# Performance work log

Hardware: AMD Instinct MI355X
Metric: run time of the kernel (lower is better)

Reference implementation:

```python
import jax, jax.numpy as jnp
import numpy as np

NBITS = 4
QN = -(2 ** (NBITS - 1))      # -8
QP = 2 ** (NBITS - 1) - 1     # 7


def grad_scale(x, scale):
    # forward: x ; backward: grad * scale (LSQ gradient scaling)
    return x * scale + jax.lax.stop_gradient(x * (1.0 - scale))


def round_pass(x):
    # straight-through estimator for round
    return x + jax.lax.stop_gradient(jnp.round(x) - x)


def lsq_quant_weight(w, alpha):
    g = 1.0 / jnp.sqrt(jnp.float32(w.size * QP))
    a = grad_scale(alpha, g)
    return round_pass(jnp.clip(w / a, QN, QP)) * a


def setup_inputs() -> dict:
    key = jax.random.key(0)
    k = jax.random.split(key, 5)
    C = 256
    N = 262144
    x = jax.random.normal(k[0], (N, C), dtype=jnp.float32)
    w1 = jax.random.normal(k[1], (C, C), dtype=jnp.float32) * 0.02
    b1 = jnp.zeros((C,), dtype=jnp.float32)
    w2 = jax.random.normal(k[2], (C, C), dtype=jnp.float32) * 0.02
    b2 = jnp.zeros((C,), dtype=jnp.float32)
    # LSQ alpha init: 2 * mean|w| / sqrt(Qp)
    alpha1 = 2.0 * jnp.mean(jnp.abs(w1)) / jnp.sqrt(jnp.float32(QP))
    alpha2 = 2.0 * jnp.mean(jnp.abs(w2)) / jnp.sqrt(jnp.float32(QP))
    return {"x": x, "w1": w1, "b1": b1, "alpha1": alpha1,
            "w2": w2, "b2": b2, "alpha2": alpha2}


def reference(x, w1, b1, alpha1, w2, b2, alpha2):
    # fc1 (4-bit LSQ weight quant) -> ReLU -> fc2 (4-bit LSQ) -> Sigmoid
    wq1 = lsq_quant_weight(w1, alpha1)
    h = jax.nn.relu(x @ wq1.T + b1)           # [N, C]
    wq2 = lsq_quant_weight(w2, alpha2)
    return jax.nn.sigmoid(h @ wq2.T + b2)     # [N, C]
```

## Files before the change

kernel.cpp:

```cpp
#include <hip/hip_runtime.h>

typedef __attribute__((ext_vector_type(4))) float f32x4;
typedef __attribute__((ext_vector_type(8))) short bf16x8;

static __device__ __forceinline__ unsigned short f2bf(float f) {
  union { float f; unsigned int u; } v;
  v.f = f;
  unsigned int r = v.u + 0x7fffu + ((v.u >> 16) & 1u);
  return (unsigned short)(r >> 16);
}

static __device__ __forceinline__ void gload16(const void* g, void* l) {
  __builtin_amdgcn_global_load_lds(
      (const __attribute__((address_space(1))) unsigned int*)g,
      (__attribute__((address_space(3))) unsigned int*)l, 16, 0, 0);
}

__global__ void lsq_pack(const float* __restrict__ w1, const float* __restrict__ a1,
                         const float* __restrict__ w2, const float* __restrict__ a2,
                         unsigned short* __restrict__ pq)
{
  int g = blockIdx.x * 256 + threadIdx.x;
  int gg = g & 8191;
  const float* w = (g < 8192) ? w1 : w2;
  float alpha = (g < 8192) ? *a1 : *a2;
  unsigned short* dst = pq + ((g < 8192) ? 0 : 65536);
  int l  = gg & 63;
  int ks = (gg >> 6) & 7;
  int cf = gg >> 9;
  int n  = cf * 16 + (l & 15);
  int kb = ks * 32 + (l >> 4) * 8;
  const float* src = w + n * 256 + kb;
  unsigned short e[8];
  #pragma unroll
  for (int j = 0; j < 8; ++j) {
    float q = src[j] / alpha;
    q = fminf(fmaxf(q, -8.f), 7.f);
    q = rintf(q) * alpha;
    e[j] = f2bf(q);
  }
  uint4 o;
  o.x = e[0] | ((unsigned)e[1] << 16);
  o.y = e[2] | ((unsigned)e[3] << 16);
  o.z = e[4] | ((unsigned)e[5] << 16);
  o.w = e[6] | ((unsigned)e[7] << 16);
  int di = (g < 8192) ? ((cf * 8 + ks) * 64 + l) : ((ks * 16 + cf) * 64 + l);
  *(uint4*)(dst + di * 8) = o;
}

__global__ __launch_bounds__(512, 2) void lsq_fused(
    const float* __restrict__ x, const unsigned short* __restrict__ pqw,
    const float* __restrict__ b1, const float* __restrict__ b2,
    float* __restrict__ out, int ntiles)
{
  __shared__ __align__(16) char w1lds[2][16384];
  __shared__ __align__(16) char w2lds[2][16384];
  __shared__ __align__(16) char hlds[8][2048];

  const int tid  = threadIdx.x;
  const int lane = tid & 63;
  const int w    = tid >> 6;
  const int l15  = lane & 15;
  const int l4   = lane >> 4;
  const int swz  = (l15 & 3) << 4;
  const char* pq1 = (const char*)pqw;
  const char* pq2 = (const char*)pqw + 131072;
  const int wb = w * 1024;
  const int lo = wb + lane * 16;

  gload16(pq1 + lo,        &w1lds[0][0]    + wb);
  gload16(pq1 + 8192 + lo, &w1lds[0][8192] + wb);
  gload16(pq2 + lo,        &w2lds[0][0]    + wb);
  gload16(pq2 + 8192 + lo, &w2lds[0][8192] + wb);
  __syncthreads();

  int gr = 0;
  for (int t = blockIdx.x; t < ntiles; t += gridDim.x) {
    const int rowbase = t * 256 + w * 32;

    bf16x8 xf[2][8];
    #pragma unroll
    for (int g = 0; g < 2; ++g) {
      const float* xp = x + (size_t)(rowbase + g * 16 + l15) * 256 + l4 * 8;
      #pragma unroll
      for (int ks = 0; ks < 8; ++ks) {
        f32x4 r0 = *(const f32x4*)(xp + ks * 32);
        f32x4 r1 = *(const f32x4*)(xp + ks * 32 + 4);
        bf16x8 b;
        #pragma unroll
        for (int j = 0; j < 4; ++j) {
          b[j]     = (short)f2bf(r0[j]);
          b[j + 4] = (short)f2bf(r1[j]);
        }
        xf[g][ks] = b;
      }
    }

    f32x4 acc2[2][16];
    const f32x4 fzero = {0.f, 0.f, 0.f, 0.f};
    #pragma unroll
    for (int g = 0; g < 2; ++g)
      #pragma unroll
      for (int c = 0; c < 16; ++c)
        acc2[g][c] = fzero;

    for (int r = 0; r < 8; ++r) {
      const int cb = gr & 1;
      const int nb = cb ^ 1;
      const int nc = (gr + 1) & 7;
      gload16(pq1 + nc * 16384 + lo,        &w1lds[nb][0]    + wb);
      gload16(pq1 + nc * 16384 + 8192 + lo, &w1lds[nb][8192] + wb);
      gload16(pq2 + nc * 16384 + lo,        &w2lds[nb][0]    + wb);
      gload16(pq2 + nc * 16384 + 8192 + lo, &w2lds[nb][8192] + wb);

      #pragma unroll
      for (int c = 0; c < 2; ++c) {
        f32x4 a0 = fzero, a1v = fzero;
        #pragma unroll
        for (int ks = 0; ks < 8; ++ks) {
          bf16x8 wf = *(const bf16x8*)(&w1lds[cb][0] + c * 8192 + ks * 1024 + lane * 16);
          a0  = __builtin_amdgcn_mfma_f32_16x16x32_bf16(wf, xf[0][ks], a0, 0, 0, 0);
          a1v = __builtin_amdgcn_mfma_f32_16x16x32_bf16(wf, xf[1][ks], a1v, 0, 0, 0);
        }
        const int cf = 2 * r + c;
        f32x4 bv = *(const f32x4*)(b1 + cf * 16 + l4 * 4);
        const int hb = (c * 32 + l4 * 8) ^ swz;
        {
          float v0 = a0[0] + bv[0]; v0 = v0 > 0.f ? v0 : 0.f;
          float v1 = a0[1] + bv[1]; v1 = v1 > 0.f ? v1 : 0.f;
          float v2 = a0[2] + bv[2]; v2 = v2 > 0.f ? v2 : 0.f;
          float v3 = a0[3] + bv[3]; v3 = v3 > 0.f ? v3 : 0.f;
          uint2 o;
          o.x = f2bf(v0) | ((unsigned)f2bf(v1) << 16);
          o.y = f2bf(v2) | ((unsigned)f2bf(v3) << 16);
          *(uint2*)(&hlds[w][0] + l15 * 64 + hb) = o;
        }
        {
          float v0 = a1v[0] + bv[0]; v0 = v0 > 0.f ? v0 : 0.f;
          float v1 = a1v[1] + bv[1]; v1 = v1 > 0.f ? v1 : 0.f;
          float v2 = a1v[2] + bv[2]; v2 = v2 > 0.f ? v2 : 0.f;
          float v3 = a1v[3] + bv[3]; v3 = v3 > 0.f ? v3 : 0.f;
          uint2 o;
          o.x = f2bf(v0) | ((unsigned)f2bf(v1) << 16);
          o.y = f2bf(v2) | ((unsigned)f2bf(v3) << 16);
          *(uint2*)(&hlds[w][0] + (16 + l15) * 64 + hb) = o;
        }
      }
      __builtin_amdgcn_sched_barrier(0);

      bf16x8 hf0 = *(const bf16x8*)(&hlds[w][0] + l15 * 64        + ((l4 * 16) ^ swz));
      bf16x8 hf1 = *(const bf16x8*)(&hlds[w][0] + (16 + l15) * 64 + ((l4 * 16) ^ swz));
      #pragma unroll
      for (int c2 = 0; c2 < 16; ++c2) {
        bf16x8 wf2 = *(const bf16x8*)(&w2lds[cb][0] + c2 * 1024 + lane * 16);
        acc2[0][c2] = __builtin_amdgcn_mfma_f32_16x16x32_bf16(wf2, hf0, acc2[0][c2], 0, 0, 0);
        acc2[1][c2] = __builtin_amdgcn_mfma_f32_16x16x32_bf16(wf2, hf1, acc2[1][c2], 0, 0, 0);
      }
      ++gr;
      __syncthreads();
    }

    #pragma unroll
    for (int g = 0; g < 2; ++g) {
      float* op = out + (size_t)(rowbase + g * 16 + l15) * 256 + l4 * 4;
      #pragma unroll
      for (int c2 = 0; c2 < 16; ++c2) {
        f32x4 bv = *(const f32x4*)(b2 + c2 * 16 + l4 * 4);
        f32x4 o;
        #pragma unroll
        for (int j = 0; j < 4; ++j) {
          float z = acc2[g][c2][j] + bv[j];
          o[j] = 1.f / (1.f + __expf(-z));
        }
        *(f32x4*)(op + c2 * 16) = o;
      }
    }
  }
}

extern "C" void kernel_launch(void* const* d_in, const int* in_sizes, int n_in,
                              void* d_out, int out_size, void* d_ws, size_t ws_size,
                              hipStream_t stream)
{
  const float* x  = (const float*)d_in[0];
  const float* w1 = (const float*)d_in[1];
  const float* b1 = (const float*)d_in[2];
  const float* a1 = (const float*)d_in[3];
  const float* w2 = (const float*)d_in[4];
  const float* b2 = (const float*)d_in[5];
  const float* a2 = (const float*)d_in[6];
  float* out = (float*)d_out;

  unsigned short* pq = (unsigned short*)d_ws;

  long long totalRows = (long long)in_sizes[0] / 256;
  int ntiles = (int)(totalRows / 256);

  lsq_pack<<<64, 256, 0, stream>>>(w1, a1, w2, a2, pq);

  int grid = ntiles < 256 ? ntiles : 256;
  lsq_fused<<<grid, 512, 0, stream>>>(x, pq, b1, b2, out, ntiles);
}
```

Before: 196.3 us.

## Prefetch next x tile into LDS and pass hidden activations via bpermute

The fused MLP kernel now stages the next 128-row x tile into a 128KB LDS buffer with swizzled async global-to-LDS loads, interleaved with the per-chunk weight loads, so HBM reads of x overlap the MFMA work of the current tile. Block size drops to 256 threads at one block per CU, and weight slots are split into a w1 slot and a w2 slot with explicit vmcnt waits and barriers. The ReLU output is moved into the second GEMM's operand layout with ds_bpermute instead of a round trip through LDS. Biases are hoisted into registers. The cost is fewer waves per CU, a large LDS footprint and a more fragile hand-written wait and barrier schedule.

```diff
diff --git a/kernel.cpp b/kernel.cpp
--- a/kernel.cpp
+++ b/kernel.cpp
@@ -2,6 +2,7 @@
 
 typedef __attribute__((ext_vector_type(4))) float f32x4;
 typedef __attribute__((ext_vector_type(8))) short bf16x8;
+typedef __attribute__((ext_vector_type(4))) unsigned int u32x4;
 
 static __device__ __forceinline__ unsigned short f2bf(float f) {
   union { float f; unsigned int u; } v;
@@ -9,12 +10,18 @@
   unsigned int r = v.u + 0x7fffu + ((v.u >> 16) & 1u);
   return (unsigned short)(r >> 16);
 }
-
+static __device__ __forceinline__ unsigned packbf(float a, float b) {
+  return (unsigned)f2bf(a) | ((unsigned)f2bf(b) << 16);
+}
 static __device__ __forceinline__ void gload16(const void* g, void* l) {
   __builtin_amdgcn_global_load_lds(
       (const __attribute__((address_space(1))) unsigned int*)g,
       (__attribute__((address_space(3))) unsigned int*)l, 16, 0, 0);
 }
+
+#define SBAR()   __builtin_amdgcn_s_barrier()
+#define SCHED0() __builtin_amdgcn_sched_barrier(0)
+#define WAITVM(N) do { asm volatile("s_waitcnt vmcnt(" #N ")" ::: "memory"); SCHED0(); } while (0)
 
 __global__ void lsq_pack(const float* __restrict__ w1, const float* __restrict__ a1,
                          const float* __restrict__ w2, const float* __restrict__ a2,
@@ -48,44 +55,50 @@
   *(uint4*)(dst + di * 8) = o;
 }
 
-__global__ __launch_bounds__(512, 2) void lsq_fused(
+__global__ __launch_bounds__(256, 1) void lsq_fused(
     const float* __restrict__ x, const unsigned short* __restrict__ pqw,
     const float* __restrict__ b1, const float* __restrict__ b2,
     float* __restrict__ out, int ntiles)
 {
-  __shared__ __align__(16) char w1lds[2][16384];
-  __shared__ __align__(16) char w2lds[2][16384];
-  __shared__ __align__(16) char hlds[8][2048];
+  __shared__ __align__(16) char lds[163840];
+  char* const xbuf  = lds;
+  char* const slot0 = lds + 131072;
+  char* const slot1 = lds + 147456;
 
   const int tid  = threadIdx.x;
   const int lane = tid & 63;
   const int w    = tid >> 6;
   const int l15  = lane & 15;
   const int l4   = lane >> 4;
-  const int swz  = (l15 & 3) << 4;
   const char* pq1 = (const char*)pqw;
   const char* pq2 = (const char*)pqw + 131072;
-  const int wb = w * 1024;
-  const int lo = wb + lane * 16;
-
-  gload16(pq1 + lo,        &w1lds[0][0]    + wb);
-  gload16(pq1 + 8192 + lo, &w1lds[0][8192] + wb);
-  gload16(pq2 + lo,        &w2lds[0][0]    + wb);
-  gload16(pq2 + 8192 + lo, &w2lds[0][8192] + wb);
-  __syncthreads();
-
-  int gr = 0;
-  for (int t = blockIdx.x; t < ntiles; t += gridDim.x) {
-    const int rowbase = t * 256 + w * 32;
-
-    bf16x8 xf[2][8];
+  const int G = gridDim.x;
+  const f32x4 fz = {0.f, 0.f, 0.f, 0.f};
+
+  f32x4 bA0[8], bA1[8], bB[16];
+  #pragma unroll
+  for (int r = 0; r < 8; ++r) {
+    bA0[r] = *(const f32x4*)(b1 + r * 32 + l4 * 4);
+    bA1[r] = *(const f32x4*)(b1 + r * 32 + 16 + l4 * 4);
+  }
+  #pragma unroll
+  for (int c2 = 0; c2 < 16; ++c2) bB[c2] = *(const f32x4*)(b2 + c2 * 16 + l4 * 4);
+
+  int idx[4];
+  #pragma unroll
+  for (int wi = 0; wi < 4; ++wi)
+    idx[wi] = (((l4 & 1) * 2 + (wi >> 1)) * 16 + l15) * 4;
+
+  bf16x8 xf[2][8];
+  auto CONVERT = [&]() {
     #pragma unroll
     for (int g = 0; g < 2; ++g) {
-      const float* xp = x + (size_t)(rowbase + g * 16 + l15) * 256 + l4 * 8;
+      const int row = w * 32 + g * 16 + l15;
+      const int swz = (l15 & 7) << 4;
       #pragma unroll
       for (int ks = 0; ks < 8; ++ks) {
-        f32x4 r0 = *(const f32x4*)(xp + ks * 32);
-        f32x4 r1 = *(const f32x4*)(xp + ks * 32 + 4);
+        f32x4 r0 = *(const f32x4*)(xbuf + row * 1024 + ((ks * 128 + l4 * 32) ^ swz));
+        f32x4 r1 = *(const f32x4*)(xbuf + row * 1024 + ((ks * 128 + l4 * 32 + 16) ^ swz));
         bf16x8 b;
         #pragma unroll
         for (int j = 0; j < 4; ++j) {
@@ -95,86 +108,130 @@
         xf[g][ks] = b;
       }
     }
-
-    f32x4 acc2[2][16];
-    const f32x4 fzero = {0.f, 0.f, 0.f, 0.f};
-    #pragma unroll
-    for (int g = 0; g < 2; ++g)
-      #pragma unroll
-      for (int c = 0; c < 16; ++c)
-        acc2[g][c] = fzero;
-
+  };
+
+  int t = blockIdx.x;
+
+  {
+    const char* xg = (const char*)x + (size_t)t * 131072;
+    #pragma unroll
+    for (int q = 0; q < 32; ++q) {
+      const int row = q * 4 + w;
+      gload16(xg + row * 1024 + ((lane * 16) ^ ((row & 7) << 4)), xbuf + row * 1024);
+    }
+    #pragma unroll
+    for (int i = 0; i < 4; ++i) {
+      const int sub = i * 4 + w;
+      gload16(pq1 + sub * 1024 + lane * 16, slot0 + sub * 1024);
+    }
+  }
+  WAITVM(0);
+  SBAR();
+  CONVERT();
+  SBAR();
+
+  f32x4 acc2[2][16];
+  #pragma unroll
+  for (int g = 0; g < 2; ++g)
+    #pragma unroll
+    for (int c2 = 0; c2 < 16; ++c2) acc2[g][c2] = fz;
+
+  for (;;) {
+    const int tn = (t + G < ntiles) ? (t + G) : t;
+    const char* xgn = (const char*)x + (size_t)tn * 131072;
+
+    #pragma unroll
     for (int r = 0; r < 8; ++r) {
-      const int cb = gr & 1;
-      const int nb = cb ^ 1;
-      const int nc = (gr + 1) & 7;
-      gload16(pq1 + nc * 16384 + lo,        &w1lds[nb][0]    + wb);
-      gload16(pq1 + nc * 16384 + 8192 + lo, &w1lds[nb][8192] + wb);
-      gload16(pq2 + nc * 16384 + lo,        &w2lds[nb][0]    + wb);
-      gload16(pq2 + nc * 16384 + 8192 + lo, &w2lds[nb][8192] + wb);
-
-      #pragma unroll
-      for (int c = 0; c < 2; ++c) {
-        f32x4 a0 = fzero, a1v = fzero;
+      bf16x8 hf[2];
+      if (r > 0) { WAITVM(2); SBAR(); }
+      #pragma unroll
+      for (int i = 0; i < 4; ++i) {
+        const int sub = i * 4 + w;
+        gload16(pq2 + r * 16384 + sub * 1024 + lane * 16, slot1 + sub * 1024);
+      }
+      SCHED0();
+      #pragma unroll
+      for (int e = 0; e < 2; ++e) {
+        const int row = (r * 4 + e) * 4 + w;
+        gload16(xgn + row * 1024 + ((lane * 16) ^ ((row & 7) << 4)), xbuf + row * 1024);
+      }
+      f32x4 aA[2][2] = {{fz, fz}, {fz, fz}};
+      #pragma unroll
+      for (int c = 0; c < 2; ++c)
         #pragma unroll
         for (int ks = 0; ks < 8; ++ks) {
-          bf16x8 wf = *(const bf16x8*)(&w1lds[cb][0] + c * 8192 + ks * 1024 + lane * 16);
-          a0  = __builtin_amdgcn_mfma_f32_16x16x32_bf16(wf, xf[0][ks], a0, 0, 0, 0);
-          a1v = __builtin_amdgcn_mfma_f32_16x16x32_bf16(wf, xf[1][ks], a1v, 0, 0, 0);
-        }
-        const int cf = 2 * r + c;
-        f32x4 bv = *(const f32x4*)(b1 + cf * 16 + l4 * 4);
-        const int hb = (c * 32 + l4 * 8) ^ swz;
-        {
-          float v0 = a0[0] + bv[0]; v0 = v0 > 0.f ? v0 : 0.f;
-          float v1 = a0[1] + bv[1]; v1 = v1 > 0.f ? v1 : 0.f;
-          float v2 = a0[2] + bv[2]; v2 = v2 > 0.f ? v2 : 0.f;
-          float v3 = a0[3] + bv[3]; v3 = v3 > 0.f ? v3 : 0.f;
-          uint2 o;
-          o.x = f2bf(v0) | ((unsigned)f2bf(v1) << 16);
-          o.y = f2bf(v2) | ((unsigned)f2bf(v3) << 16);
-          *(uint2*)(&hlds[w][0] + l15 * 64 + hb) = o;
-        }
-        {
-          float v0 = a1v[0] + bv[0]; v0 = v0 > 0.f ? v0 : 0.f;
-          float v1 = a1v[1] + bv[1]; v1 = v1 > 0.f ? v1 : 0.f;
-          float v2 = a1v[2] + bv[2]; v2 = v2 > 0.f ? v2 : 0.f;
-          float v3 = a1v[3] + bv[3]; v3 = v3 > 0.f ? v3 : 0.f;
-          uint2 o;
-          o.x = f2bf(v0) | ((unsigned)f2bf(v1) << 16);
-          o.y = f2bf(v2) | ((unsigned)f2bf(v3) << 16);
-          *(uint2*)(&hlds[w][0] + (16 + l15) * 64 + hb) = o;
-        }
-      }
-      __builtin_amdgcn_sched_barrier(0);
-
-      bf16x8 hf0 = *(const bf16x8*)(&hlds[w][0] + l15 * 64        + ((l4 * 16) ^ swz));
-      bf16x8 hf1 = *(const bf16x8*)(&hlds[w][0] + (16 + l15) * 64 + ((l4 * 16) ^ swz));
+          bf16x8 wf = *(const bf16x8*)(slot0 + c * 8192 + ks * 1024 + lane * 16);
+          aA[c][0] = __builtin_amdgcn_mfma_f32_16x16x32_bf16(wf, xf[0][ks], aA[c][0], 0, 0, 0);
+          aA[c][1] = __builtin_amdgcn_mfma_f32_16x16x32_bf16(wf, xf[1][ks], aA[c][1], 0, 0, 0);
+        }
+      #pragma unroll
+      for (int g = 0; g < 2; ++g) {
+        f32x4 v0, v1;
+        #pragma unroll
+        for (int j = 0; j < 4; ++j) {
+          v0[j] = fmaxf(aA[0][g][j] + bA0[r][j], 0.f);
+          v1[j] = fmaxf(aA[1][g][j] + bA1[r][j], 0.f);
+        }
+        const unsigned D0 = packbf(v0[0], v0[1]);
+        const unsigned D1 = packbf(v0[2], v0[3]);
+        const unsigned D2 = packbf(v1[0], v1[1]);
+        const unsigned D3 = packbf(v1[2], v1[3]);
+        unsigned hd[4];
+        #pragma unroll
+        for (int wi = 0; wi < 4; ++wi) {
+          const int p0 = __builtin_amdgcn_ds_bpermute(idx[wi], (int)((wi & 1) ? D1 : D0));
+          const int p1 = __builtin_amdgcn_ds_bpermute(idx[wi], (int)((wi & 1) ? D3 : D2));
+          hd[wi] = (l4 >= 2) ? (unsigned)p1 : (unsigned)p0;
+        }
+        union { u32x4 u; bf16x8 v; } cv;
+        cv.u[0] = hd[0]; cv.u[1] = hd[1]; cv.u[2] = hd[2]; cv.u[3] = hd[3];
+        hf[g] = cv.v;
+      }
+      WAITVM(2); SBAR();
+      #pragma unroll
+      for (int i = 0; i < 4; ++i) {
+        const int sub = i * 4 + w;
+        gload16(pq1 + ((r + 1) & 7) * 16384 + sub * 1024 + lane * 16, slot0 + sub * 1024);
+      }
+      SCHED0();
+      #pragma unroll
+      for (int e = 0; e < 2; ++e) {
+        const int row = (r * 4 + 2 + e) * 4 + w;
+        gload16(xgn + row * 1024 + ((lane * 16) ^ ((row & 7) << 4)), xbuf + row * 1024);
+      }
       #pragma unroll
       for (int c2 = 0; c2 < 16; ++c2) {
-        bf16x8 wf2 = *(const bf16x8*)(&w2lds[cb][0] + c2 * 1024 + lane * 16);
-        acc2[0][c2] = __builtin_amdgcn_mfma_f32_16x16x32_bf16(wf2, hf0, acc2[0][c2], 0, 0, 0);
-        acc2[1][c2] = __builtin_amdgcn_mfma_f32_16x16x32_bf16(wf2, hf1, acc2[1][c2], 0, 0, 0);
-      }
-      ++gr;
-      __syncthreads();
-    }
-
-    #pragma unroll
-    for (int g = 0; g < 2; ++g) {
-      float* op = out + (size_t)(rowbase + g * 16 + l15) * 256 + l4 * 4;
-      #pragma unroll
-      for (int c2 = 0; c2 < 16; ++c2) {
-        f32x4 bv = *(const f32x4*)(b2 + c2 * 16 + l4 * 4);
-        f32x4 o;
-        #pragma unroll
-        for (int j = 0; j < 4; ++j) {
-          float z = acc2[g][c2][j] + bv[j];
-          o[j] = 1.f / (1.f + __expf(-z));
-        }
-        *(f32x4*)(op + c2 * 16) = o;
-      }
-    }
+        bf16x8 wf2 = *(const bf16x8*)(slot1 + c2 * 1024 + lane * 16);
+        acc2[0][c2] = __builtin_amdgcn_mfma_f32_16x16x32_bf16(wf2, hf[0], acc2[0][c2], 0, 0, 0);
+        acc2[1][c2] = __builtin_amdgcn_mfma_f32_16x16x32_bf16(wf2, hf[1], acc2[1][c2], 0, 0, 0);
+      }
+    }
+
+    WAITVM(0); SBAR();
+    const bool last = (t + G >= ntiles);
+    if (!last) { CONVERT(); }
+    SBAR();
+
+    {
+      const size_t rb = (size_t)t * 128 + w * 32;
+      #pragma unroll
+      for (int g = 0; g < 2; ++g) {
+        float* op = out + (rb + g * 16 + l15) * 256 + l4 * 4;
+        #pragma unroll
+        for (int c2 = 0; c2 < 16; ++c2) {
+          f32x4 o;
+          #pragma unroll
+          for (int j = 0; j < 4; ++j) {
+            const float z = acc2[g][c2][j] + bB[c2][j];
+            o[j] = 1.f / (1.f + __expf(-z));
+          }
+          *(f32x4*)(op + c2 * 16) = o;
+          acc2[g][c2] = fz;
+        }
+      }
+    }
+    if (last) break;
+    t = tn;
   }
 }
 
@@ -190,14 +247,15 @@
   const float* b2 = (const float*)d_in[5];
   const float* a2 = (const float*)d_in[6];
   float* out = (float*)d_out;
+  (void)ws_size;
 
   unsigned short* pq = (unsigned short*)d_ws;
 
   long long totalRows = (long long)in_sizes[0] / 256;
-  int ntiles = (int)(totalRows / 256);
+  int ntiles = (int)(totalRows / 128);
 
   lsq_pack<<<64, 256, 0, stream>>>(w1, a1, w2, a2, pq);
 
   int grid = ntiles < 256 ? ntiles : 256;
-  lsq_fused<<<grid, 512, 0, stream>>>(x, pq, b1, b2, out, ntiles);
-}
+  lsq_fused<<<grid, 256, 0, stream>>>(x, pq, b1, b2, out, ntiles);
+}
```

New measurement: 290.6 us. +48.1%, slower.
